# Optimization experiments

Hardware: AMD Instinct MI355X
Metric: run time of the kernel (lower is better)

Reference implementation:

```python
import jax, jax.numpy as jnp
import numpy as np

N = 100000
E = 1600000
IN_DIM = 128
HID = 64
HEADS = 4
OUT = HID // HEADS  # 16
LAYERS = 3
NEG_SLOPE = 0.2
LN_EPS = 1e-5


def setup_inputs() -> dict:
    key = jax.random.key(0)
    ks = jax.random.split(key, 12)
    x = jax.random.normal(ks[0], (N, IN_DIM), dtype=jnp.float32)
    edge_index = jax.random.randint(ks[1], (2, E), 0, N, dtype=jnp.int32)
    s = 0.05
    Win = jax.random.normal(ks[2], (IN_DIM, HID), dtype=jnp.float32) * s
    bin_ = jnp.zeros((HID,), dtype=jnp.float32)
    Wg = jax.random.normal(ks[3], (LAYERS, HID, HEADS * OUT), dtype=jnp.float32) * s
    att_src = jax.random.normal(ks[4], (LAYERS, HEADS, OUT), dtype=jnp.float32) * s
    att_dst = jax.random.normal(ks[5], (LAYERS, HEADS, OUT), dtype=jnp.float32) * s
    bg = jnp.zeros((LAYERS, HID), dtype=jnp.float32)
    ln_g = jnp.ones((LAYERS, HID), dtype=jnp.float32)
    ln_b = jnp.zeros((LAYERS, HID), dtype=jnp.float32)
    Wout = jax.random.normal(ks[6], (HID, 1), dtype=jnp.float32) * s
    bout = jnp.zeros((1,), dtype=jnp.float32)
    return {"x": x, "edge_index": edge_index, "Win": Win, "bin_": bin_,
            "Wg": Wg, "att_src": att_src, "att_dst": att_dst, "bg": bg,
            "ln_g": ln_g, "ln_b": ln_b, "Wout": Wout, "bout": bout}


def _gat_layer(x, src, dst, W, a_s, a_d, b):
    # x: [N, HID]; linear transform then split heads
    h = (x @ W).reshape(N, HEADS, OUT)                       # [N,H,C]
    alpha_s = jnp.einsum('nhc,hc->nh', h, a_s)               # [N,H]
    alpha_d = jnp.einsum('nhc,hc->nh', h, a_d)               # [N,H]
    e = alpha_s[src] + alpha_d[dst]                          # [E',H]
    e = jnp.where(e > 0, e, NEG_SLOPE * e)                   # LeakyReLU(0.2)
    # segment softmax over destination node
    m = jax.ops.segment_max(e, dst, num_segments=N)          # [N,H]
    ee = jnp.exp(e - m[dst])
    z = jax.ops.segment_sum(ee, dst, num_segments=N)         # [N,H]
    alpha = ee / (z[dst] + 1e-16)                            # [E',H]
    msg = alpha[:, :, None] * h[src]                         # [E',H,C]
    out = jax.ops.segment_sum(msg, dst, num_segments=N)      # [N,H,C]
    return out.reshape(N, HID) + b


def _layer_norm(x, g, b):
    mu = jnp.mean(x, axis=-1, keepdims=True)
    var = jnp.mean(jnp.square(x - mu), axis=-1, keepdims=True)
    return (x - mu) * jax.lax.rsqrt(var + LN_EPS) * g + b


def reference(x, edge_index, Win, bin_, Wg, att_src, att_dst, bg, ln_g, ln_b, Wout, bout):
    # add self loops (PyG GATConv default)
    loops = jnp.arange(N, dtype=edge_index.dtype)
    src = jnp.concatenate([edge_index[0], loops])
    dst = jnp.concatenate([edge_index[1], loops])
    h = jax.nn.relu(x @ Win + bin_)                          # input_proj + ReLU
    for i in range(LAYERS):
        res = h
        h = _gat_layer(h, src, dst, Wg[i], att_src[i], att_dst[i], bg[i])
        h = _layer_norm(h, ln_g[i], ln_b[i])
        h = jax.nn.relu(h)
        h = h + res                                          # dropout is identity in eval
    out = h @ Wout + bout                                    # [N,1]
    return out.reshape(-1)
```

## Files before the change

### kernel.cpp

```cpp
#include <hip/hip_runtime.h>
#include <hip/hip_bf16.h>

#define N_NODES 100000
#define E_EDGES 1600000
#define IN_DIM  128
#define HID     64
#define HEADS   4
#define NEG_SLOPE 0.2f
#define LN_EPS  1e-5f
#define LOG2E   1.4426950408889634f

#define BUCK_SHIFT 7
#define NODES_PER_BUCK 128
#define NBUCK ((N_NODES + NODES_PER_BUCK - 1) / NODES_PER_BUCK)
#define NBUCK_PAD 1024
#define PART_CHUNK 8192
#define HIST_BLOCKS 256

typedef float f2v __attribute__((ext_vector_type(2)));

__device__ __forceinline__ float bflo(unsigned u) { return __uint_as_float(u << 16); }
__device__ __forceinline__ float bfhi(unsigned u) { return __uint_as_float(u & 0xffff0000u); }
__device__ __forceinline__ f2v unp2(unsigned u) {
    f2v r; r.x = __uint_as_float(u << 16); r.y = __uint_as_float(u & 0xffff0000u); return r;
}
__device__ __forceinline__ unsigned packbf2(float a, float b) {
    unsigned ua = __float_as_uint(a), ub = __float_as_uint(b);
    ua += 0x7fffu + ((ua >> 16) & 1u);
    ub += 0x7fffu + ((ub >> 16) & 1u);
    return (ua >> 16) | (ub & 0xffff0000u);
}
__device__ __forceinline__ float lrexp2(float e) {
    return __builtin_amdgcn_exp2f(fmaxf(e, NEG_SLOPE * e));
}

__global__ __launch_bounds__(256) void k_in_proj_fused(
        const float* __restrict__ x, const float* __restrict__ W,
        const float* __restrict__ bias,
        const float* __restrict__ W2g, const float* __restrict__ as_w,
        const float* __restrict__ ad_w,
        float* __restrict__ h, unsigned* __restrict__ hlb,
        float* __restrict__ as_o, float* __restrict__ ad_o) {
    __shared__ float Xs[32][132];
    __shared__ float Ws[128][64];
    __shared__ float W2[64][64];
    int t = threadIdx.x;
    const float4* W4 = (const float4*)W;
    float4* Ws4 = (float4*)&Ws[0][0];
    #pragma unroll
    for (int i = 0; i < 8; ++i) Ws4[t + 256 * i] = W4[t + 256 * i];
    const float4* W24 = (const float4*)W2g;
    float4* W2s4 = (float4*)&W2[0][0];
    #pragma unroll
    for (int i = 0; i < 4; ++i) W2s4[t + 256 * i] = W24[t + 256 * i];
    int base = blockIdx.x * 32;
    const float4* X4 = (const float4*)(x + (size_t)base * IN_DIM);
    #pragma unroll
    for (int i = 0; i < 4; ++i) {
        int f = t + 256 * i;
        int row = f >> 5, col4 = f & 31;
        ((float4*)&Xs[row][0])[col4] = X4[f];
    }
    __syncthreads();
    int r = t >> 4;
    int c = (t & 15) * 4;
    float4 bb = *(const float4*)(bias + c);
    float4 acc0 = bb, acc1 = bb;
    #pragma unroll 8
    for (int k = 0; k < 128; ++k) {
        float a0 = Xs[r][k];
        float a1 = Xs[r + 16][k];
        float4 b = *(const float4*)&Ws[k][c];
        acc0.x += a0 * b.x; acc0.y += a0 * b.y; acc0.z += a0 * b.z; acc0.w += a0 * b.w;
        acc1.x += a1 * b.x; acc1.y += a1 * b.y; acc1.z += a1 * b.z; acc1.w += a1 * b.w;
    }
    acc0.x = fmaxf(acc0.x, 0.f); acc0.y = fmaxf(acc0.y, 0.f);
    acc0.z = fmaxf(acc0.z, 0.f); acc0.w = fmaxf(acc0.w, 0.f);
    acc1.x = fmaxf(acc1.x, 0.f); acc1.y = fmaxf(acc1.y, 0.f);
    acc1.z = fmaxf(acc1.z, 0.f); acc1.w = fmaxf(acc1.w, 0.f);
    *(float4*)(h + (size_t)(base + r) * HID + c) = acc0;
    *(float4*)(h + (size_t)(base + r + 16) * HID + c) = acc1;
    __syncthreads();
    float (*H2)[68] = (float(*)[68])Xs;
    *(float4*)&H2[r][c] = acc0;
    *(float4*)&H2[r + 16][c] = acc1;
    __syncthreads();
    float4 s0v = {0.f,0.f,0.f,0.f}, s1v = {0.f,0.f,0.f,0.f};
    #pragma unroll 8
    for (int k = 0; k < 64; ++k) {
        float a0 = H2[r][k];
        float a1 = H2[r + 16][k];
        float4 b = *(const float4*)&W2[k][c];
        s0v.x += a0 * b.x; s0v.y += a0 * b.y; s0v.z += a0 * b.z; s0v.w += a0 * b.w;
        s1v.x += a1 * b.x; s1v.y += a1 * b.y; s1v.z += a1 * b.z; s1v.w += a1 * b.w;
    }
    uint2 p0, p1;
    p0.x = packbf2(s0v.x, s0v.y); p0.y = packbf2(s0v.z, s0v.w);
    p1.x = packbf2(s1v.x, s1v.y); p1.y = packbf2(s1v.z, s1v.w);
    ((uint2*)hlb)[(size_t)(base + r) * 16 + (c >> 2)] = p0;
    ((uint2*)hlb)[(size_t)(base + r + 16) * 16 + (c >> 2)] = p1;
    float4 A = *(const float4*)(as_w + c);
    float4 D = *(const float4*)(ad_w + c);
    A.x *= LOG2E; A.y *= LOG2E; A.z *= LOG2E; A.w *= LOG2E;
    D.x *= LOG2E; D.y *= LOG2E; D.z *= LOG2E; D.w *= LOG2E;
    float s0 = s0v.x * A.x + s0v.y * A.y + s0v.z * A.z + s0v.w * A.w;
    float d0 = s0v.x * D.x + s0v.y * D.y + s0v.z * D.z + s0v.w * D.w;
    float s1 = s1v.x * A.x + s1v.y * A.y + s1v.z * A.z + s1v.w * A.w;
    float d1 = s1v.x * D.x + s1v.y * D.y + s1v.z * D.z + s1v.w * D.w;
    #pragma unroll
    for (int off = 1; off < 4; off <<= 1) {
        s0 += __shfl_xor(s0, off); d0 += __shfl_xor(d0, off);
        s1 += __shfl_xor(s1, off); d1 += __shfl_xor(d1, off);
    }
    if ((t & 3) == 0) {
        int head = (t & 15) >> 2;
        as_o[(size_t)(base + r) * HEADS + head] = s0;
        ad_o[(size_t)(base + r) * HEADS + head] = d0;
        as_o[(size_t)(base + r + 16) * HEADS + head] = s1;
        ad_o[(size_t)(base + r + 16) * HEADS + head] = d1;
    }
}

__global__ __launch_bounds__(256) void k_gat_lin(
        const float* __restrict__ h, const float* __restrict__ W,
        const float* __restrict__ as_w, const float* __restrict__ ad_w,
        unsigned* __restrict__ hlb, float* __restrict__ as_o, float* __restrict__ ad_o) {
    __shared__ float Xs[32][68];
    __shared__ float Ws[64][64];
    int t = threadIdx.x;
    const float4* W4 = (const float4*)W;
    float4* Ws4 = (float4*)&Ws[0][0];
    #pragma unroll
    for (int i = 0; i < 4; ++i) Ws4[t + 256 * i] = W4[t + 256 * i];
    int base = blockIdx.x * 32;
    const float4* X4 = (const float4*)(h + (size_t)base * HID);
    #pragma unroll
    for (int i = 0; i < 2; ++i) {
        int f = t + 256 * i;
        int row = f >> 4, col4 = f & 15;
        ((float4*)&Xs[row][0])[col4] = X4[f];
    }
    __syncthreads();
    int r = t >> 4;
    int c = (t & 15) * 4;
    float4 acc0 = {0.f, 0.f, 0.f, 0.f}, acc1 = {0.f, 0.f, 0.f, 0.f};
    #pragma unroll 8
    for (int k = 0; k < 64; ++k) {
        float a0 = Xs[r][k];
        float a1 = Xs[r + 16][k];
        float4 b = *(const float4*)&Ws[k][c];
        acc0.x += a0 * b.x; acc0.y += a0 * b.y; acc0.z += a0 * b.z; acc0.w += a0 * b.w;
        acc1.x += a1 * b.x; acc1.y += a1 * b.y; acc1.z += a1 * b.z; acc1.w += a1 * b.w;
    }
    uint2 p0, p1;
    p0.x = packbf2(acc0.x, acc0.y); p0.y = packbf2(acc0.z, acc0.w);
    p1.x = packbf2(acc1.x, acc1.y); p1.y = packbf2(acc1.z, acc1.w);
    ((uint2*)hlb)[(size_t)(base + r) * 16 + (c >> 2)] = p0;
    ((uint2*)hlb)[(size_t)(base + r + 16) * 16 + (c >> 2)] = p1;
    float4 A = *(const float4*)(as_w + c);
    float4 D = *(const float4*)(ad_w + c);
    A.x *= LOG2E; A.y *= LOG2E; A.z *= LOG2E; A.w *= LOG2E;
    D.x *= LOG2E; D.y *= LOG2E; D.z *= LOG2E; D.w *= LOG2E;
    float s0 = acc0.x * A.x + acc0.y * A.y + acc0.z * A.z + acc0.w * A.w;
    float d0 = acc0.x * D.x + acc0.y * D.y + acc0.z * D.z + acc0.w * D.w;
    float s1 = acc1.x * A.x + acc1.y * A.y + acc1.z * A.z + acc1.w * A.w;
    float d1 = acc1.x * D.x + acc1.y * D.y + acc1.z * D.z + acc1.w * D.w;
    #pragma unroll
    for (int off = 1; off < 4; off <<= 1) {
        s0 += __shfl_xor(s0, off); d0 += __shfl_xor(d0, off);
        s1 += __shfl_xor(s1, off); d1 += __shfl_xor(d1, off);
    }
    if ((t & 3) == 0) {
        int head = (t & 15) >> 2;
        as_o[(size_t)(base + r) * HEADS + head] = s0;
        ad_o[(size_t)(base + r) * HEADS + head] = d0;
        as_o[(size_t)(base + r + 16) * HEADS + head] = s1;
        ad_o[(size_t)(base + r + 16) * HEADS + head] = d1;
    }
}

__global__ __launch_bounds__(256) void k_bhist_scan(
        const int* __restrict__ dstp, int* __restrict__ bcnt,
        int* __restrict__ done, int* __restrict__ bbase, int* __restrict__ bcur) {
    __shared__ int c[NBUCK_PAD];
    __shared__ int tsum[256];
    __shared__ int lastFlag;
    int t = threadIdx.x;
    for (int i = t; i < NBUCK_PAD; i += 256) c[i] = 0;
    __syncthreads();
    for (int i = blockIdx.x * 256 + t; i < E_EDGES; i += gridDim.x * 256)
        atomicAdd(&c[dstp[i] >> BUCK_SHIFT], 1);
    __syncthreads();
    for (int i = t; i < NBUCK_PAD; i += 256) {
        int v = c[i];
        if (v) atomicAdd(bcnt + i, v);
    }
    __threadfence();
    if (t == 0) lastFlag = (atomicAdd(done, 1) == (int)gridDim.x - 1);
    __syncthreads();
    if (!lastFlag) return;
    int v0 = bcnt[t * 4 + 0], v1 = bcnt[t * 4 + 1];
    int v2 = bcnt[t * 4 + 2], v3 = bcnt[t * 4 + 3];
    int local = v0 + v1 + v2 + v3;
    tsum[t] = local;
    __syncthreads();
    for (int off = 1; off < 256; off <<= 1) {
        int u = (t >= off) ? tsum[t - off] : 0;
        __syncthreads();
        tsum[t] += u;
        __syncthreads();
    }
    int p = tsum[t] - local;
    bbase[t * 4 + 0] = p; bcur[t * 4 + 0] = p; p += v0;
    bbase[t * 4 + 1] = p; bcur[t * 4 + 1] = p; p += v1;
    bbase[t * 4 + 2] = p; bcur[t * 4 + 2] = p; p += v2;
    bbase[t * 4 + 3] = p; bcur[t * 4 + 3] = p; p += v3;
    if (t == 255) bbase[NBUCK_PAD] = p;
}

__global__ __launch_bounds__(256) void k_part(const int* __restrict__ srcp,
                                              const int* __restrict__ dstp,
                                              int* __restrict__ bcur,
                                              unsigned* __restrict__ ebuf) {
    __shared__ int cnt[NBUCK_PAD];
    __shared__ int gbase[NBUCK_PAD];
    int t = threadIdx.x;
    for (int i = t; i < NBUCK_PAD; i += 256) cnt[i] = 0;
    int e0 = blockIdx.x * PART_CHUNK;
    int e1 = min(e0 + PART_CHUNK, E_EDGES);
    __syncthreads();
    for (int i = e0 + t; i < e1; i += 256)
        atomicAdd(&cnt[dstp[i] >> BUCK_SHIFT], 1);
    __syncthreads();
    for (int b = t; b < NBUCK_PAD; b += 256) {
        int c = cnt[b];
        gbase[b] = c ? atomicAdd(bcur + b, c) : 0;
        cnt[b] = 0;
    }
    __syncthreads();
    for (int i = e0 + t; i < e1; i += 256) {
        int d = dstp[i];
        int b = d >> BUCK_SHIFT;
        int pos = gbase[b] + atomicAdd(&cnt[b], 1);
        ebuf[pos] = (unsigned)srcp[i] | ((unsigned)(d & 127) << 17);
    }
}

__global__ __launch_bounds__(256) void k_fin(const int* __restrict__ bbase,
                                             const unsigned* __restrict__ ebuf,
                                             int* __restrict__ row,
                                             int* __restrict__ ssrc) {
    __shared__ int cnt[NODES_PER_BUCK];
    __shared__ int sc[NODES_PER_BUCK];
    __shared__ int rbase[NODES_PER_BUCK];
    int t = threadIdx.x;
    int b = blockIdx.x;
    int start = bbase[b], end = bbase[b + 1];
    int nb0 = b << BUCK_SHIFT;
    if (t < NODES_PER_BUCK) cnt[t] = 0;
    __syncthreads();
    for (int i = start + t; i < end; i += 256)
        atomicAdd(&cnt[ebuf[i] >> 17], 1);
    __syncthreads();
    if (t < NODES_PER_BUCK) sc[t] = cnt[t];
    __syncthreads();
    for (int off = 1; off < NODES_PER_BUCK; off <<= 1) {
        int v = (t < NODES_PER_BUCK && t >= off) ? sc[t - off] : 0;
        __syncthreads();
        if (t < NODES_PER_BUCK) sc[t] += v;
        __syncthreads();
    }
    if (t < NODES_PER_BUCK) {
        int rb = start + sc[t] - cnt[t];
        rbase[t] = rb;
        int n = nb0 + t;
        if (n < N_NODES) row[n] = rb;
        cnt[t] = 0;
    }
    if (b == NBUCK - 1 && t == 0) row[N_NODES] = E_EDGES;
    __syncthreads();
    for (int i = start + t; i < end; i += 256) {
        unsigned p = ebuf[i];
        int l = (int)(p >> 17);
        int slot = rbase[l] + atomicAdd(&cnt[l], 1);
        ssrc[slot] = (int)(p & 0x1FFFFu);
    }
}

__global__ __launch_bounds__(256) void k_gat_agg(
        const int* __restrict__ row, const int* __restrict__ ssrc,
        const float* __restrict__ as_, const float* __restrict__ ad_,
        const unsigned* __restrict__ hlb, const float* __restrict__ hres,
        const float* __restrict__ bg, const float* __restrict__ g,
        const float* __restrict__ b, float* __restrict__ hout,
        const float* __restrict__ Wout, const float* __restrict__ bout,
        float* __restrict__ out, int last) {
    int gid = blockIdx.x * blockDim.x + threadIdx.x;
    int n = gid >> 6;
    if (n >= N_NODES) return;
    int lane = threadIdx.x & 63;
    int grp = lane >> 3;
    int q   = lane & 7;
    int head = q >> 1;
    const char* hlbc = (const char*)hlb;
    const char* asc  = (const char*)as_;
    unsigned qb = (unsigned)q * 16u;
    unsigned hb = (unsigned)head * 4u;
    float adh = ad_[n * 4 + head];
    f2v acc[4];
    #pragma unroll
    for (int i = 0; i < 4; ++i) { acc[i].x = 0.f; acc[i].y = 0.f; }
    float z = 0.f;
    if (grp == 0) {
        float w = lrexp2(*(const float*)(asc + ((unsigned)n * 16u + hb)) + adh);
        f2v w2; w2.x = w; w2.y = w;
        uint4 u = *(const uint4*)(hlbc + ((unsigned)n * 128u + qb));
        acc[0] = w2 * unp2(u.x);
        acc[1] = w2 * unp2(u.y);
        acc[2] = w2 * unp2(u.z);
        acc[3] = w2 * unp2(u.w);
        z = w;
    }
    int j = row[n] + grp;
    int jend = row[n + 1];
    for (; j + 8 < jend; j += 16) {
        unsigned s0 = (unsigned)ssrc[j], s1 = (unsigned)ssrc[j + 8];
        float wa = lrexp2(*(const float*)(asc + (s0 * 16u + hb)) + adh);
        float wb = lrexp2(*(const float*)(asc + (s1 * 16u + hb)) + adh);
        uint4 ua = *(const uint4*)(hlbc + (s0 * 128u + qb));
        uint4 ub = *(const uint4*)(hlbc + (s1 * 128u + qb));
        f2v wa2; wa2.x = wa; wa2.y = wa;
        f2v wb2; wb2.x = wb; wb2.y = wb;
        acc[0] += wa2 * unp2(ua.x); acc[1] += wa2 * unp2(ua.y);
        acc[2] += wa2 * unp2(ua.z); acc[3] += wa2 * unp2(ua.w);
        acc[0] += wb2 * unp2(ub.x); acc[1] += wb2 * unp2(ub.y);
        acc[2] += wb2 * unp2(ub.z); acc[3] += wb2 * unp2(ub.w);
        z += wa + wb;
    }
    if (j < jend) {
        unsigned s0 = (unsigned)ssrc[j];
        float wa = lrexp2(*(const float*)(asc + (s0 * 16u + hb)) + adh);
        uint4 ua = *(const uint4*)(hlbc + (s0 * 128u + qb));
        f2v wa2; wa2.x = wa; wa2.y = wa;
        acc[0] += wa2 * unp2(ua.x); acc[1] += wa2 * unp2(ua.y);
        acc[2] += wa2 * unp2(ua.z); acc[3] += wa2 * unp2(ua.w);
        z += wa;
    }
    #pragma unroll
    for (int i = 0; i < 4; ++i) {
        acc[i].x += __shfl_xor(acc[i].x, 8);
        acc[i].y += __shfl_xor(acc[i].y, 8);
        acc[i].x += __shfl_xor(acc[i].x, 16);
        acc[i].y += __shfl_xor(acc[i].y, 16);
        acc[i].x += __shfl_xor(acc[i].x, 32);
        acc[i].y += __shfl_xor(acc[i].y, 32);
    }
    z += __shfl_xor(z, 8); z += __shfl_xor(z, 16); z += __shfl_xor(z, 32);
    float rz = 1.f / (z + 1e-16f);
    float4 bg0 = ((const float4*)bg)[2 * q];
    float4 bg1 = ((const float4*)bg)[2 * q + 1];
    float v[8];
    v[0] = acc[0].x * rz + bg0.x; v[1] = acc[0].y * rz + bg0.y;
    v[2] = acc[1].x * rz + bg0.z; v[3] = acc[1].y * rz + bg0.w;
    v[4] = acc[2].x * rz + bg1.x; v[5] = acc[2].y * rz + bg1.y;
    v[6] = acc[3].x * rz + bg1.z; v[7] = acc[3].y * rz + bg1.w;
    float ssum = 0.f;
    #pragma unroll
    for (int i = 0; i < 8; ++i) ssum += v[i];
    #pragma unroll
    for (int off = 1; off < 8; off <<= 1) ssum += __shfl_xor(ssum, off);
    float mu = ssum * (1.f / 64.f);
    float vs = 0.f;
    #pragma unroll
    for (int i = 0; i < 8; ++i) { v[i] -= mu; vs += v[i] * v[i]; }
    #pragma unroll
    for (int off = 1; off < 8; off <<= 1) vs += __shfl_xor(vs, off);
    float rstd = rsqrtf(vs * (1.f / 64.f) + LN_EPS);
    float4 g0 = ((const float4*)g)[2 * q];
    float4 g1 = ((const float4*)g)[2 * q + 1];
    float4 b0 = ((const float4*)b)[2 * q];
    float4 b1 = ((const float4*)b)[2 * q + 1];
    float4 h0 = ((const float4*)hres)[(size_t)n * 16 + 2 * q];
    float4 h1 = ((const float4*)hres)[(size_t)n * 16 + 2 * q + 1];
    float y[8];
    y[0] = fmaxf(v[0] * rstd * g0.x + b0.x, 0.f) + h0.x;
    y[1] = fmaxf(v[1] * rstd * g0.y + b0.y, 0.f) + h0.y;
    y[2] = fmaxf(v[2] * rstd * g0.z + b0.z, 0.f) + h0.z;
    y[3] = fmaxf(v[3] * rstd * g0.w + b0.w, 0.f) + h0.w;
    y[4] = fmaxf(v[4] * rstd * g1.x + b1.x, 0.f) + h1.x;
    y[5] = fmaxf(v[5] * rstd * g1.y + b1.y, 0.f) + h1.y;
    y[6] = fmaxf(v[6] * rstd * g1.z + b1.z, 0.f) + h1.z;
    y[7] = fmaxf(v[7] * rstd * g1.w + b1.w, 0.f) + h1.w;
    if (!last) {
        if (grp == 0) {
            float4 o0; o0.x = y[0]; o0.y = y[1]; o0.z = y[2]; o0.w = y[3];
            float4 o1; o1.x = y[4]; o1.y = y[5]; o1.z = y[6]; o1.w = y[7];
            ((float4*)hout)[(size_t)n * 16 + 2 * q] = o0;
            ((float4*)hout)[(size_t)n * 16 + 2 * q + 1] = o1;
        }
    } else {
        float4 w0 = ((const float4*)Wout)[2 * q];
        float4 w1 = ((const float4*)Wout)[2 * q + 1];
        float pp = y[0] * w0.x + y[1] * w0.y + y[2] * w0.z + y[3] * w0.w
                 + y[4] * w1.x + y[5] * w1.y + y[6] * w1.z + y[7] * w1.w;
        #pragma unroll
        for (int off = 1; off < 8; off <<= 1) pp += __shfl_xor(pp, off);
        if (lane == 0) out[n] = pp + bout[0];
    }
}

extern "C" void kernel_launch(void* const* d_in, const int* in_sizes, int n_in,
                              void* d_out, int out_size, void* d_ws, size_t ws_size,
                              hipStream_t stream) {
    const float* x     = (const float*)d_in[0];
    const int*   ei    = (const int*)  d_in[1];
    const float* Win   = (const float*)d_in[2];
    const float* bin_  = (const float*)d_in[3];
    const float* Wg    = (const float*)d_in[4];
    const float* att_s = (const float*)d_in[5];
    const float* att_d = (const float*)d_in[6];
    const float* bg    = (const float*)d_in[7];
    const float* lng   = (const float*)d_in[8];
    const float* lnb   = (const float*)d_in[9];
    const float* Wout  = (const float*)d_in[10];
    const float* bout  = (const float*)d_in[11];
    float* out = (float*)d_out;

    float* hA   = (float*)d_ws;
    float* hC   = hA + (size_t)N_NODES * 64;
    unsigned* hlb = (unsigned*)(hC + (size_t)N_NODES * 64);
    float* as_  = (float*)(hlb + (size_t)N_NODES * 32);
    float* ad_  = as_ + (size_t)N_NODES * 4;
    int* row    = (int*)(ad_ + (size_t)N_NODES * 4);
    int* bcnt   = row + (N_NODES + 1);
    int* done   = bcnt + NBUCK_PAD;
    int* bbase  = done + 1;
    int* bcur   = bbase + (NBUCK_PAD + 1);
    int* ssrc   = bcur + NBUCK_PAD;
    unsigned* ebuf = (unsigned*)(ssrc + E_EDGES);

    const int* srcp = ei;
    const int* dstp = ei + E_EDGES;

    hipMemsetAsync(bcnt, 0, (NBUCK_PAD + 1) * sizeof(int), stream);
    k_bhist_scan<<<HIST_BLOCKS, 256, 0, stream>>>(dstp, bcnt, done, bbase, bcur);
    k_part<<<(E_EDGES + PART_CHUNK - 1) / PART_CHUNK, 256, 0, stream>>>(srcp, dstp, bcur, ebuf);
    k_fin<<<NBUCK, 256, 0, stream>>>(bbase, ebuf, row, ssrc);

    k_in_proj_fused<<<N_NODES / 32, 256, 0, stream>>>(
        x, Win, bin_, Wg, att_s, att_d, hA, hlb, as_, ad_);

    const int aggBlocks = (N_NODES * 64 + 255) / 256;
    for (int L = 0; L < 3; ++L) {
        if (L > 0) {
            k_gat_lin<<<N_NODES / 32, 256, 0, stream>>>(hA, Wg + L * 64 * 64,
                                                att_s + L * 64, att_d + L * 64,
                                                hlb, as_, ad_);
        }
        k_gat_agg<<<aggBlocks, 256, 0, stream>>>(row, ssrc, as_, ad_, hlb, hA,
                                                 bg + L * 64, lng + L * 64, lnb + L * 64,
                                                 hC, Wout, bout, out, (L == 2) ? 1 : 0);
        float* t = hA; hA = hC; hC = t;
    }
}
```

Baseline: 353.1 us.

## Map one node per 8-lane group in GAT aggregation instead of one per wavefront

The aggregation kernel now assigns each destination node to an 8-lane group, so one wavefront handles 8 nodes, instead of spreading a single node's edges across all 64 lanes. Each group walks its node's edge list serially, two edges at a time, which removes the cross-group shuffle reductions and the idle lanes on low-degree nodes. The grid shrinks eightfold to match. In exchange, per-lane serial work grows and varies with node degree, which can cause divergence inside a wavefront.

```diff
diff --git a/kernel.cpp b/kernel.cpp
--- a/kernel.cpp
+++ b/kernel.cpp
@@ -19,8 +19,6 @@
 
 typedef float f2v __attribute__((ext_vector_type(2)));
 
-__device__ __forceinline__ float bflo(unsigned u) { return __uint_as_float(u << 16); }
-__device__ __forceinline__ float bfhi(unsigned u) { return __uint_as_float(u & 0xffff0000u); }
 __device__ __forceinline__ f2v unp2(unsigned u) {
     f2v r; r.x = __uint_as_float(u << 16); r.y = __uint_as_float(u & 0xffff0000u); return r;
 }
@@ -296,45 +294,40 @@
         const float* __restrict__ Wout, const float* __restrict__ bout,
         float* __restrict__ out, int last) {
     int gid = blockIdx.x * blockDim.x + threadIdx.x;
-    int n = gid >> 6;
-    if (n >= N_NODES) return;
     int lane = threadIdx.x & 63;
     int grp = lane >> 3;
     int q   = lane & 7;
+    int n = (gid >> 6) * 8 + grp;
+    if (n >= N_NODES) return;
     int head = q >> 1;
     const char* hlbc = (const char*)hlb;
     const char* asc  = (const char*)as_;
+    unsigned nb = (unsigned)n;
     unsigned qb = (unsigned)q * 16u;
     unsigned hb = (unsigned)head * 4u;
-    float adh = ad_[n * 4 + head];
-    f2v acc[4];
-    #pragma unroll
-    for (int i = 0; i < 4; ++i) { acc[i].x = 0.f; acc[i].y = 0.f; }
-    float z = 0.f;
-    if (grp == 0) {
-        float w = lrexp2(*(const float*)(asc + ((unsigned)n * 16u + hb)) + adh);
-        f2v w2; w2.x = w; w2.y = w;
-        uint4 u = *(const uint4*)(hlbc + ((unsigned)n * 128u + qb));
-        acc[0] = w2 * unp2(u.x);
-        acc[1] = w2 * unp2(u.y);
-        acc[2] = w2 * unp2(u.z);
-        acc[3] = w2 * unp2(u.w);
-        z = w;
-    }
-    int j = row[n] + grp;
+    float adh = *(const float*)((const char*)ad_ + (nb * 16u + hb));
+    float w = lrexp2(*(const float*)(asc + (nb * 16u + hb)) + adh);
+    f2v w2; w2.x = w; w2.y = w;
+    uint4 u = *(const uint4*)(hlbc + (nb * 128u + qb));
+    f2v acc0 = w2 * unp2(u.x);
+    f2v acc1 = w2 * unp2(u.y);
+    f2v acc2 = w2 * unp2(u.z);
+    f2v acc3 = w2 * unp2(u.w);
+    float z = w;
+    int j = row[n];
     int jend = row[n + 1];
-    for (; j + 8 < jend; j += 16) {
-        unsigned s0 = (unsigned)ssrc[j], s1 = (unsigned)ssrc[j + 8];
+    for (; j + 1 < jend; j += 2) {
+        unsigned s0 = (unsigned)ssrc[j], s1 = (unsigned)ssrc[j + 1];
         float wa = lrexp2(*(const float*)(asc + (s0 * 16u + hb)) + adh);
         float wb = lrexp2(*(const float*)(asc + (s1 * 16u + hb)) + adh);
         uint4 ua = *(const uint4*)(hlbc + (s0 * 128u + qb));
         uint4 ub = *(const uint4*)(hlbc + (s1 * 128u + qb));
         f2v wa2; wa2.x = wa; wa2.y = wa;
         f2v wb2; wb2.x = wb; wb2.y = wb;
-        acc[0] += wa2 * unp2(ua.x); acc[1] += wa2 * unp2(ua.y);
-        acc[2] += wa2 * unp2(ua.z); acc[3] += wa2 * unp2(ua.w);
-        acc[0] += wb2 * unp2(ub.x); acc[1] += wb2 * unp2(ub.y);
-        acc[2] += wb2 * unp2(ub.z); acc[3] += wb2 * unp2(ub.w);
+        acc0 += wa2 * unp2(ua.x); acc1 += wa2 * unp2(ua.y);
+        acc2 += wa2 * unp2(ua.z); acc3 += wa2 * unp2(ua.w);
+        acc0 += wb2 * unp2(ub.x); acc1 += wb2 * unp2(ub.y);
+        acc2 += wb2 * unp2(ub.z); acc3 += wb2 * unp2(ub.w);
         z += wa + wb;
     }
     if (j < jend) {
@@ -342,28 +335,18 @@
         float wa = lrexp2(*(const float*)(asc + (s0 * 16u + hb)) + adh);
         uint4 ua = *(const uint4*)(hlbc + (s0 * 128u + qb));
         f2v wa2; wa2.x = wa; wa2.y = wa;
-        acc[0] += wa2 * unp2(ua.x); acc[1] += wa2 * unp2(ua.y);
-        acc[2] += wa2 * unp2(ua.z); acc[3] += wa2 * unp2(ua.w);
+        acc0 += wa2 * unp2(ua.x); acc1 += wa2 * unp2(ua.y);
+        acc2 += wa2 * unp2(ua.z); acc3 += wa2 * unp2(ua.w);
         z += wa;
     }
-    #pragma unroll
-    for (int i = 0; i < 4; ++i) {
-        acc[i].x += __shfl_xor(acc[i].x, 8);
-        acc[i].y += __shfl_xor(acc[i].y, 8);
-        acc[i].x += __shfl_xor(acc[i].x, 16);
-        acc[i].y += __shfl_xor(acc[i].y, 16);
-        acc[i].x += __shfl_xor(acc[i].x, 32);
-        acc[i].y += __shfl_xor(acc[i].y, 32);
-    }
-    z += __shfl_xor(z, 8); z += __shfl_xor(z, 16); z += __shfl_xor(z, 32);
     float rz = 1.f / (z + 1e-16f);
     float4 bg0 = ((const float4*)bg)[2 * q];
     float4 bg1 = ((const float4*)bg)[2 * q + 1];
     float v[8];
-    v[0] = acc[0].x * rz + bg0.x; v[1] = acc[0].y * rz + bg0.y;
-    v[2] = acc[1].x * rz + bg0.z; v[3] = acc[1].y * rz + bg0.w;
-    v[4] = acc[2].x * rz + bg1.x; v[5] = acc[2].y * rz + bg1.y;
-    v[6] = acc[3].x * rz + bg1.z; v[7] = acc[3].y * rz + bg1.w;
+    v[0] = acc0.x * rz + bg0.x; v[1] = acc0.y * rz + bg0.y;
+    v[2] = acc1.x * rz + bg0.z; v[3] = acc1.y * rz + bg0.w;
+    v[4] = acc2.x * rz + bg1.x; v[5] = acc2.y * rz + bg1.y;
+    v[6] = acc3.x * rz + bg1.z; v[7] = acc3.y * rz + bg1.w;
     float ssum = 0.f;
     #pragma unroll
     for (int i = 0; i < 8; ++i) ssum += v[i];
@@ -392,12 +375,10 @@
     y[6] = fmaxf(v[6] * rstd * g1.z + b1.z, 0.f) + h1.z;
     y[7] = fmaxf(v[7] * rstd * g1.w + b1.w, 0.f) + h1.w;
     if (!last) {
-        if (grp == 0) {
-            float4 o0; o0.x = y[0]; o0.y = y[1]; o0.z = y[2]; o0.w = y[3];
-            float4 o1; o1.x = y[4]; o1.y = y[5]; o1.z = y[6]; o1.w = y[7];
-            ((float4*)hout)[(size_t)n * 16 + 2 * q] = o0;
-            ((float4*)hout)[(size_t)n * 16 + 2 * q + 1] = o1;
-        }
+        float4 o0; o0.x = y[0]; o0.y = y[1]; o0.z = y[2]; o0.w = y[3];
+        float4 o1; o1.x = y[4]; o1.y = y[5]; o1.z = y[6]; o1.w = y[7];
+        ((float4*)hout)[(size_t)n * 16 + 2 * q] = o0;
+        ((float4*)hout)[(size_t)n * 16 + 2 * q + 1] = o1;
     } else {
         float4 w0 = ((const float4*)Wout)[2 * q];
         float4 w1 = ((const float4*)Wout)[2 * q + 1];
@@ -405,7 +386,7 @@
                  + y[4] * w1.x + y[5] * w1.y + y[6] * w1.z + y[7] * w1.w;
         #pragma unroll
         for (int off = 1; off < 8; off <<= 1) pp += __shfl_xor(pp, off);
-        if (lane == 0) out[n] = pp + bout[0];
+        if (q == 0) out[n] = pp + bout[0];
     }
 }
 
@@ -450,7 +431,7 @@
     k_in_proj_fused<<<N_NODES / 32, 256, 0, stream>>>(
         x, Win, bin_, Wg, att_s, att_d, hA, hlb, as_, ad_);
 
-    const int aggBlocks = (N_NODES * 64 + 255) / 256;
+    const int aggBlocks = (N_NODES + 31) / 32;
     for (int L = 0; L < 3; ++L) {
         if (L > 0) {
             k_gat_lin<<<N_NODES / 32, 256, 0, stream>>>(hA, Wg + L * 64 * 64,
```

Measured after the change: 316.2 us. 1.12x faster.
